# Kernel optimization log

Measured on AMD Instinct MI355X. Metric: run time of the kernel, lower is better.

## Reference

```python
import jax, jax.numpy as jnp
import numpy as np

B, L, D, H, K = 8, 200, 256, 8, 20
HS = D // H


def setup_inputs() -> dict:
    key = jax.random.key(0)
    ks = jax.random.split(key, 12)
    def xavier(k, shape):
        fan_in, fan_out = shape[1], shape[0]
        lim = np.sqrt(2.0) * np.sqrt(6.0 / (fan_in + fan_out))  # gain=relu
        return jax.random.uniform(k, shape, jnp.float32, -lim, lim)
    return {
        "seqs": jax.random.normal(ks[0], (B, L, D), jnp.float32),
        "attention_mask": jax.random.bernoulli(ks[1], 0.3, (L, L)),
        "time_matrices": jax.random.normal(ks[2], (B, L, L, D), jnp.float32),
        "conv1_w": xavier(ks[3], (D, D)),
        "conv1_b": jnp.zeros((D,), jnp.float32),
        "conv2_w": xavier(ks[4], (D, D)),
        "conv2_b": jnp.zeros((D,), jnp.float32),
        "W_w": jax.random.normal(ks[5], (D, D), jnp.float32) * (1.0 / np.sqrt(D)),
        "W_b": jnp.zeros((D,), jnp.float32),
        "ln_gamma": jnp.ones((D,), jnp.float32),
        "ln_beta": jnp.zeros((D,), jnp.float32),
    }


def _to_heads(x):
    # torch.cat(torch.split(x, HS, dim=-1), dim=0): [B,L,D] -> [H*B,L,HS], index h*B+b
    return jnp.concatenate(jnp.split(x, H, axis=-1), axis=0)


def _from_heads(x):
    # inverse: [H*B,L,HS] -> [B,L,D]
    return jnp.concatenate(jnp.split(x, H, axis=0), axis=-1)


def reference(seqs, attention_mask, time_matrices, conv1_w, conv1_b,
              conv2_w, conv2_b, W_w, W_b, ln_gamma, ln_beta):
    # 1x1 Conv1d == per-token linear
    a_ = seqs @ conv1_w.T + conv1_b
    b_ = seqs @ conv2_w.T + conv2_b
    a = _to_heads(a_)                    # [HB, L, HS]
    b = _to_heads(b_)                    # [HB, L, HS]
    ti = jnp.concatenate(jnp.split(time_matrices, H, axis=3), axis=0)  # [HB, L, L, HS]

    # attention scores: QK^T + time interaction
    att = jnp.einsum('bqh,bkh->bqk', a, b) + jnp.einsum('bqkh,bqh->bqk', ti, a)
    a_2 = jnp.linalg.norm(a, axis=-1)[..., None]              # [HB, L, 1]
    b_t_2 = jnp.linalg.norm(b[:, None, :, :] + ti, axis=-1)   # [HB, L, L]
    raw_graph = att / (a_2 * b_t_2 + 1e-6)

    attn_mask = jnp.broadcast_to(attention_mask[None], raw_graph.shape)
    raw_graph = jnp.where(attn_mask, 0.0, raw_graph)

    # top-K per row, symmetric binary mask (vectorized scatter)
    _, idx = jax.lax.top_k(raw_graph, K)                      # [HB, L, K]
    HB = raw_graph.shape[0]
    bi = jnp.arange(HB)[:, None, None]
    ri = jnp.arange(L)[None, :, None]
    mask = jnp.zeros_like(raw_graph).at[bi, ri, idx].set(1.0)
    mask = mask.at[bi, idx, ri].set(1.0)
    mask = jax.lax.stop_gradient(mask)

    sparse_graph = jnp.where(attn_mask, 0.0, raw_graph * mask)

    seqs_h = _to_heads(seqs @ W_w.T + W_b)                    # [HB, L, HS]
    outputs = sparse_graph @ seqs_h                           # [HB, L, HS]
    time_outputs = jnp.einsum('bqk,bqkh->bqh', sparse_graph, ti)

    outputs = _from_heads(outputs)                            # [B, L, D]
    time_outputs = _from_heads(time_outputs)                  # [B, L, D]

    # LayerNorm(eps=1e-8), biased variance (torch semantics)
    mu = outputs.mean(-1, keepdims=True)
    var = ((outputs - mu) ** 2).mean(-1, keepdims=True)
    ln = (outputs - mu) / jnp.sqrt(var + 1e-8) * ln_gamma + ln_beta
    return ln, time_outputs
```

## Files before the change

kernel.cpp:

```cpp
#include <hip/hip_runtime.h>
#include <hip/hip_bf16.h>

#define B_  8
#define L_  200
#define D_  256
#define H_  8
#define HS_ 32
#define K_  20
#define BL_ 1600
#define G_  64
#define MW_ 7
#define NEG_INF (-3.402823466e38f)

__device__ __forceinline__ float bf2f(unsigned short u){
  return __uint_as_float(((unsigned int)u) << 16);
}
__device__ __forceinline__ unsigned short f2bf(float f){
  unsigned int x = __float_as_uint(f);
  unsigned int r = (x + 0x7fffu + ((x >> 16) & 1u)) >> 16;
  return (unsigned short)r;
}
__device__ __forceinline__ void up2(unsigned int u, float& lo, float& hi){
  lo = __uint_as_float(u << 16);
  hi = __uint_as_float(u & 0xffff0000u);
}

__device__ __forceinline__ float loadf(const void* base, size_t i, int fp){
  return fp ? ((const float*)base)[i] : bf2f(((const unsigned short*)base)[i]);
}
__device__ __forceinline__ void load8f(const void* base, size_t i, int fp, float f[8]){
  if (fp){
    const float4* p = (const float4*)((const float*)base + i);
    float4 x = p[0], y = p[1];
    f[0]=x.x; f[1]=x.y; f[2]=x.z; f[3]=x.w; f[4]=y.x; f[5]=y.y; f[6]=y.z; f[7]=y.w;
  } else {
    uint4 v = *(const uint4*)((const unsigned short*)base + i);
    up2(v.x,f[0],f[1]); up2(v.y,f[2],f[3]); up2(v.z,f[4],f[5]); up2(v.w,f[6],f[7]);
  }
}
__device__ __forceinline__ int mask_at(const void* am, int i, int mk){
  switch(mk){
    case 0:  return ((const int*)am)[i] != 0;
    case 1:  return ((const unsigned char*)am)[i] != 0;
    case 2:  return ((const unsigned int*)am)[i] != 0;
    default: return ((const unsigned short*)am)[i] != 0;
  }
}
__device__ __forceinline__ void storef(void* base, size_t i, int fp, float v){
  if (fp) ((float*)base)[i] = v; else ((unsigned short*)base)[i] = f2bf(v);
}

__global__ __launch_bounds__(256) void k_detect(
    const unsigned short* __restrict__ seqs, const unsigned int* __restrict__ am,
    int* __restrict__ flags)
{
  int t = threadIdx.x;
  __shared__ int r[5];
  if (t < 5) r[t] = 0;
  __syncthreads();

  int bad = 0;
  for (int i = t; i < 4096; i += 256){
    unsigned e = (seqs[i] >> 7) & 0xFFu;
    if (e >= 160u) bad++;
  }
  int vi = 0, vb = 0, vf = 0, vh = 0;
  for (int i = t; i < 1024; i += 256){
    unsigned w = am[i];
    if (w == 0u) continue;
    if (w == 1u) vi++;
    else if (w == 0x3F800000u) vf++;
    else if (w == 0x00003F80u || w == 0x3F803F80u) vh++;
    else if ((w & 0xFEFEFEFEu) == 0u) vb++;
    else vb++;
  }
  atomicAdd(&r[0], bad); atomicAdd(&r[1], vi); atomicAdd(&r[2], vb);
  atomicAdd(&r[3], vf);  atomicAdd(&r[4], vh);
  __syncthreads();
  if (t == 0){
    flags[0] = (r[0] > 32) ? 1 : 0;
    int kind;
    if (r[2] > r[1] && r[2] > r[3] + r[4]) kind = 1;
    else if (r[4] > 0)                     kind = 3;
    else if (r[3] > r[1])                  kind = 2;
    else                                   kind = 0;
    flags[1] = kind;
  }
}

__global__ __launch_bounds__(256) void kz_zero(unsigned int* __restrict__ p, int n){
  int i = blockIdx.x * 256 + threadIdx.x;
  if (i < n) p[i] = 0u;
}

__global__ __launch_bounds__(256) void k1_linear(
    const void* __restrict__ seqs,
    const void* __restrict__ w1, const void* __restrict__ b1,
    const void* __restrict__ w2, const void* __restrict__ b2,
    const void* __restrict__ w3, const void* __restrict__ b3,
    const int* __restrict__ flags,
    float* __restrict__ da, float* __restrict__ db, float* __restrict__ dsh)
{
  int fp = flags[0];
  int bid = blockIdx.x;
  int m  = bid / 400;
  int rb = (bid % 400) * 4;
  const void* w; const void* bias; float* dst;
  if (m == 0)      { w = w1; bias = b1; dst = da;  }
  else if (m == 1) { w = w2; bias = b2; dst = db;  }
  else             { w = w3; bias = b3; dst = dsh; }

  __shared__ float s4[4][D_];
  int t = threadIdx.x;
  for (int l = t; l < 4 * D_; l += 256){
    int rr = l >> 8, c = l & 255;
    s4[rr][c] = loadf(seqs, (size_t)(rb + rr) * D_ + c, fp);
  }
  __syncthreads();

  float acc[4];
  float bv = loadf(bias, t, fp);
  #pragma unroll
  for (int rr = 0; rr < 4; rr++) acc[rr] = bv;

  for (int c8 = 0; c8 < 32; c8++){
    float wf[8];
    load8f(w, (size_t)t * D_ + c8 * 8, fp, wf);
    #pragma unroll
    for (int rr = 0; rr < 4; rr++){
      const float* sf = &s4[rr][c8 * 8];
      #pragma unroll
      for (int i = 0; i < 8; i++) acc[rr] += sf[i] * wf[i];
    }
  }
  #pragma unroll
  for (int rr = 0; rr < 4; rr++)
    dst[(size_t)(rb + rr) * D_ + t] = acc[rr];
}

__global__ __launch_bounds__(256) void k2_rawtopk(
    const float* __restrict__ a_, const float* __restrict__ b_,
    const void* __restrict__ tm, const void* __restrict__ am,
    const int* __restrict__ flags, unsigned int* __restrict__ maskw)
{
  int fp = flags[0], mk = flags[1];
  int bid = blockIdx.x;
  int bb = bid / L_;
  int q  = bid - bb * L_;
  int t = threadIdx.x;
  int h = t >> 5, j = t & 31;

  __shared__ float a_sh[D_];
  __shared__ float b_sh[32 * 257];
  __shared__ float raw_sh[8 * 208];

  a_sh[t] = a_[(size_t)(bb * L_ + q) * D_ + t];
  __syncthreads();

  float areg[HS_];
  #pragma unroll
  for (int e = 0; e < HS_; e++) areg[e] = a_sh[h * HS_ + e];
  float a2 = 0.f;
  #pragma unroll
  for (int e = 0; e < HS_; e++) a2 += areg[e] * areg[e];
  a2 = sqrtf(a2);

  const int amrow = q * L_;

  for (int tile = 0; tile < 7; tile++){
    __syncthreads();
    for (int l = t; l < 32 * D_; l += 256){
      int row = l >> 8;
      int col = l & 255;
      int k = tile * 32 + row;
      float v = 0.f;
      if (k < L_) v = b_[(size_t)(bb * L_ + k) * D_ + col];
      b_sh[row * 257 + col] = v;
    }
    __syncthreads();

    int k = tile * 32 + j;
    if (k < L_){
      size_t pbase = ((size_t)(bb * L_ + q) * L_ + k) * D_ + h * HS_;
      const float* brow = &b_sh[j * 257 + h * HS_];
      float p1 = 0.f, p2 = 0.f;
      #pragma unroll
      for (int e8 = 0; e8 < 4; e8++){
        float tf[8];
        load8f(tm, pbase + e8 * 8, fp, tf);
        #pragma unroll
        for (int i = 0; i < 8; i++){
          float s = brow[e8 * 8 + i] + tf[i];
          p1 += areg[e8 * 8 + i] * s;
          p2 += s * s;
        }
      }
      float r = p1 / (a2 * sqrtf(p2) + 1e-6f);
      if (mask_at(am, amrow + k, mk)) r = 0.f;
      raw_sh[h * 208 + k] = r;
    }
  }
  __syncthreads();

  int wv = t >> 6, lane = t & 63;
  for (int hh = 2 * wv; hh <= 2 * wv + 1; hh++){
    const float* r = &raw_sh[hh * 208];
    int g = hh * B_ + bb;

    float v0 = (lane       < L_) ? r[lane]       : NEG_INF;
    float v1 = (lane + 64  < L_) ? r[lane + 64]  : NEG_INF;
    float v2 = (lane + 128 < L_) ? r[lane + 128] : NEG_INF;
    float v3 = (lane + 192 < L_) ? r[lane + 192] : NEG_INF;

    for (int it = 0; it < K_; it++){
      float bv = v0; int bi = lane;
      if (v1 > bv){ bv = v1; bi = lane + 64;  }
      if (v2 > bv){ bv = v2; bi = lane + 128; }
      if (v3 > bv){ bv = v3; bi = lane + 192; }
      #pragma unroll
      for (int off = 1; off < 64; off <<= 1){
        float ov = __shfl_xor(bv, off);
        int   oi = __shfl_xor(bi, off);
        if (ov > bv || (ov == bv && oi < bi)){ bv = ov; bi = oi; }
      }
      if (bi == lane)            v0 = NEG_INF;
      else if (bi == lane + 64)  v1 = NEG_INF;
      else if (bi == lane + 128) v2 = NEG_INF;
      else if (bi == lane + 192) v3 = NEG_INF;
      if (lane == 0){
        atomicOr(&maskw[((size_t)g * L_ + q)  * MW_ + (bi >> 5)], 1u << (bi & 31));
        atomicOr(&maskw[((size_t)g * L_ + bi) * MW_ + (q  >> 5)], 1u << (q  & 31));
      }
    }
  }
}

__global__ __launch_bounds__(256) void k3_gatherln(
    const float* __restrict__ a_, const float* __restrict__ b_,
    const float* __restrict__ sh_, const void* __restrict__ tm,
    const void* __restrict__ am, const unsigned int* __restrict__ maskw,
    const void* __restrict__ gamma, const void* __restrict__ beta,
    const int* __restrict__ flags, void* __restrict__ out)
{
  int fp = flags[0], mk = flags[1];
  int bid = blockIdx.x;
  int bb = bid / L_;
  int q  = bid - bb * L_;
  int t = threadIdx.x;

  __shared__ float a_sh[D_];
  __shared__ float s_a2[8];
  __shared__ int   s_k[8][200];
  __shared__ float s_v[8][200];
  __shared__ int   s_cnt[8];
  __shared__ float red[8];

  a_sh[t] = a_[(size_t)(bb * L_ + q) * D_ + t];
  __syncthreads();
  if (t < 8){
    float s = 0.f;
    #pragma unroll
    for (int e = 0; e < HS_; e++){ float d = a_sh[t * HS_ + e]; s += d * d; }
    s_a2[t] = sqrtf(s);
  }
  __syncthreads();

  int wv = t >> 6, lane = t & 63;
  for (int hh = 2 * wv; hh <= 2 * wv + 1; hh++){
    int g = hh * B_ + bb;
    const unsigned int* mrow = &maskw[((size_t)g * L_ + q) * MW_];
    int cnt = 0;
    #pragma unroll
    for (int c = 0; c < 4; c++){
      int k = c * 64 + lane;
      bool sel = (k < L_) && ((mrow[k >> 5] >> (k & 31)) & 1u) && !mask_at(am, q * L_ + k, mk);
      unsigned long long bal = __ballot(sel);
      int pos = __popcll(bal & ((1ull << lane) - 1ull));
      if (sel) s_k[hh][cnt + pos] = k;
      cnt += __popcll(bal);
    }
    if (lane == 0) s_cnt[hh] = cnt;
    float a2 = s_a2[hh];
    for (int i = lane; i < cnt; i += 64){
      int k = s_k[hh][i];
      size_t pbase = ((size_t)(bb * L_ + q) * L_ + k) * D_ + hh * HS_;
      const float4* b4 = (const float4*)(b_ + (size_t)(bb * L_ + k) * D_ + hh * HS_);
      float p1 = 0.f, p2 = 0.f;
      #pragma unroll
      for (int e8 = 0; e8 < 4; e8++){
        float tf[8];
        load8f(tm, pbase + e8 * 8, fp, tf);
        float4 bv0 = b4[e8 * 2], bv1 = b4[e8 * 2 + 1];
        float bf[8] = {bv0.x, bv0.y, bv0.z, bv0.w, bv1.x, bv1.y, bv1.z, bv1.w};
        #pragma unroll
        for (int i2 = 0; i2 < 8; i2++){
          float s = bf[i2] + tf[i2];
          p1 += a_sh[hh * HS_ + e8 * 8 + i2] * s;
          p2 += s * s;
        }
      }
      s_v[hh][i] = p1 / (a2 * sqrtf(p2) + 1e-6f);
    }
  }
  __syncthreads();

  int h = t >> 5, hs = t & 31;
  int cnt = s_cnt[h];
  float acc_o = 0.f, acc_t = 0.f;
  const size_t tmrow = (size_t)(bb * L_ + q) * L_ * D_;
  for (int i = 0; i < cnt; i++){
    int k = s_k[h][i];
    float v = s_v[h][i];
    acc_o += v * sh_[(size_t)(bb * L_ + k) * D_ + h * HS_ + hs];
    acc_t += v * loadf(tm, tmrow + (size_t)k * D_ + h * HS_ + hs, fp);
  }
  size_t orow = (size_t)(bb * L_ + q) * D_;
  storef(out, (size_t)409600 + orow + t, fp, acc_t);

  float s = acc_o;
  #pragma unroll
  for (int off = 1; off < 64; off <<= 1) s += __shfl_xor(s, off);
  if (lane == 0) red[wv] = s;
  __syncthreads();
  float mean = (red[0] + red[1] + red[2] + red[3]) * (1.f / 256.f);

  float d = acc_o - mean;
  float s2 = d * d;
  #pragma unroll
  for (int off = 1; off < 64; off <<= 1) s2 += __shfl_xor(s2, off);
  if (lane == 0) red[4 + wv] = s2;
  __syncthreads();
  float var = (red[4] + red[5] + red[6] + red[7]) * (1.f / 256.f);

  float y = d * (1.f / sqrtf(var + 1e-8f)) * loadf(gamma, t, fp) + loadf(beta, t, fp);
  storef(out, orow + t, fp, y);
}

extern "C" void kernel_launch(void* const* d_in, const int* in_sizes, int n_in,
                              void* d_out, int out_size, void* d_ws, size_t ws_size,
                              hipStream_t stream) {
  const void* seqs = d_in[0];
  const void* am   = d_in[1];
  const void* tm   = d_in[2];
  const void* w1   = d_in[3];
  const void* b1   = d_in[4];
  const void* w2   = d_in[5];
  const void* b2   = d_in[6];
  const void* w3   = d_in[7];
  const void* b3   = d_in[8];
  const void* lng  = d_in[9];
  const void* lnb  = d_in[10];

  float* ws = (float*)d_ws;
  int*   flags = (int*)ws;
  float* a_    = ws + 16;
  float* b_    = ws + 16 + 409600;
  float* sh_   = ws + 16 + 819200;
  unsigned int* maskw = (unsigned int*)(ws + 16 + 1228800);

  k_detect   <<<1,   256, 0, stream>>>((const unsigned short*)seqs, (const unsigned int*)am, flags);
  kz_zero    <<<350, 256, 0, stream>>>(maskw, G_ * L_ * MW_);
  k1_linear  <<<1200, 256, 0, stream>>>(seqs, w1, b1, w2, b2, w3, b3, flags, a_, b_, sh_);
  k2_rawtopk <<<BL_, 256, 0, stream>>>(a_, b_, tm, am, flags, maskw);
  k3_gatherln<<<BL_, 256, 0, stream>>>(a_, b_, sh_, tm, am, maskw, lng, lnb, flags, d_out);
}
```

Before: 705.6 us.

## Read b and time rows directly with coalesced loads and cache raw scores for gather

The score kernel no longer stages b tiles in shared memory. Each group of four lanes now covers one head's 32 channels for a key, and the partial sums are combined with shuffles, so both the time-matrix and b reads become contiguous rows. The full raw-score matrix is also written to workspace, letting the gather kernel look up selected scores instead of re-reading time_matrices to recompute them. This adds a roughly 10 MB score buffer, which is only used when the workspace is large enough.

```diff
diff --git a/kernel.cpp b/kernel.cpp
--- a/kernel.cpp
+++ b/kernel.cpp
@@ -141,66 +141,74 @@
 __global__ __launch_bounds__(256) void k2_rawtopk(
     const float* __restrict__ a_, const float* __restrict__ b_,
     const void* __restrict__ tm, const void* __restrict__ am,
-    const int* __restrict__ flags, unsigned int* __restrict__ maskw)
+    const int* __restrict__ flags, unsigned int* __restrict__ maskw,
+    float* __restrict__ rawg)
 {
   int fp = flags[0], mk = flags[1];
   int bid = blockIdx.x;
   int bb = bid / L_;
   int q  = bid - bb * L_;
   int t = threadIdx.x;
-  int h = t >> 5, j = t & 31;
-
-  __shared__ float a_sh[D_];
-  __shared__ float b_sh[32 * 257];
+  int rsub = t >> 5;
+  int cg   = t & 31;
+  int c0   = cg * 8;
+  int h    = cg >> 2;
+
   __shared__ float raw_sh[8 * 208];
 
-  a_sh[t] = a_[(size_t)(bb * L_ + q) * D_ + t];
-  __syncthreads();
-
-  float areg[HS_];
-  #pragma unroll
-  for (int e = 0; e < HS_; e++) areg[e] = a_sh[h * HS_ + e];
-  float a2 = 0.f;
-  #pragma unroll
-  for (int e = 0; e < HS_; e++) a2 += areg[e] * areg[e];
-  a2 = sqrtf(a2);
-
+  float areg[8];
+  const float* arow = a_ + (size_t)(bb * L_ + q) * D_;
+  {
+    const float4* a4 = (const float4*)(arow + c0);
+    float4 x = a4[0], y = a4[1];
+    areg[0]=x.x; areg[1]=x.y; areg[2]=x.z; areg[3]=x.w;
+    areg[4]=y.x; areg[5]=y.y; areg[6]=y.z; areg[7]=y.w;
+  }
+  float a2;
+  {
+    float s = 0.f;
+    #pragma unroll
+    for (int e = 0; e < 8; e++) s += areg[e] * areg[e];
+    s += __shfl_xor(s, 1);
+    s += __shfl_xor(s, 2);
+    a2 = sqrtf(s);
+  }
+
+  const size_t tmbase = (size_t)(bb * L_ + q) * L_ * D_;
+  const float* bbase  = b_ + (size_t)bb * L_ * D_;
   const int amrow = q * L_;
 
-  for (int tile = 0; tile < 7; tile++){
-    __syncthreads();
-    for (int l = t; l < 32 * D_; l += 256){
-      int row = l >> 8;
-      int col = l & 255;
-      int k = tile * 32 + row;
-      float v = 0.f;
-      if (k < L_) v = b_[(size_t)(bb * L_ + k) * D_ + col];
-      b_sh[row * 257 + col] = v;
-    }
-    __syncthreads();
-
-    int k = tile * 32 + j;
-    if (k < L_){
-      size_t pbase = ((size_t)(bb * L_ + q) * L_ + k) * D_ + h * HS_;
-      const float* brow = &b_sh[j * 257 + h * HS_];
-      float p1 = 0.f, p2 = 0.f;
-      #pragma unroll
-      for (int e8 = 0; e8 < 4; e8++){
-        float tf[8];
-        load8f(tm, pbase + e8 * 8, fp, tf);
-        #pragma unroll
-        for (int i = 0; i < 8; i++){
-          float s = brow[e8 * 8 + i] + tf[i];
-          p1 += areg[e8 * 8 + i] * s;
-          p2 += s * s;
-        }
-      }
+  for (int k0 = 0; k0 < L_; k0 += 8){
+    int k = k0 + rsub;
+    float tf[8];
+    load8f(tm, tmbase + (size_t)k * D_ + c0, fp, tf);
+    const float4* b4 = (const float4*)(bbase + (size_t)k * D_ + c0);
+    float4 bv0 = b4[0], bv1 = b4[1];
+    float bf[8] = {bv0.x, bv0.y, bv0.z, bv0.w, bv1.x, bv1.y, bv1.z, bv1.w};
+    float p1 = 0.f, p2 = 0.f;
+    #pragma unroll
+    for (int i = 0; i < 8; i++){
+      float sv = bf[i] + tf[i];
+      p1 += areg[i] * sv;
+      p2 += sv * sv;
+    }
+    p1 += __shfl_xor(p1, 1); p2 += __shfl_xor(p2, 1);
+    p1 += __shfl_xor(p1, 2); p2 += __shfl_xor(p2, 2);
+    if ((cg & 3) == 0){
       float r = p1 / (a2 * sqrtf(p2) + 1e-6f);
       if (mask_at(am, amrow + k, mk)) r = 0.f;
       raw_sh[h * 208 + k] = r;
     }
   }
   __syncthreads();
+
+  if (rawg){
+    #pragma unroll
+    for (int hh2 = 0; hh2 < 8; hh2++){
+      if (t < L_)
+        rawg[((size_t)(hh2 * B_ + bb) * L_ + q) * L_ + t] = raw_sh[hh2 * 208 + t];
+    }
+  }
 
   int wv = t >> 6, lane = t & 63;
   for (int hh = 2 * wv; hh <= 2 * wv + 1; hh++){
@@ -240,7 +248,8 @@
     const float* __restrict__ sh_, const void* __restrict__ tm,
     const void* __restrict__ am, const unsigned int* __restrict__ maskw,
     const void* __restrict__ gamma, const void* __restrict__ beta,
-    const int* __restrict__ flags, void* __restrict__ out)
+    const int* __restrict__ flags, const float* __restrict__ rawg,
+    void* __restrict__ out)
 {
   int fp = flags[0], mk = flags[1];
   int bid = blockIdx.x;
@@ -280,26 +289,33 @@
       cnt += __popcll(bal);
     }
     if (lane == 0) s_cnt[hh] = cnt;
-    float a2 = s_a2[hh];
-    for (int i = lane; i < cnt; i += 64){
-      int k = s_k[hh][i];
-      size_t pbase = ((size_t)(bb * L_ + q) * L_ + k) * D_ + hh * HS_;
-      const float4* b4 = (const float4*)(b_ + (size_t)(bb * L_ + k) * D_ + hh * HS_);
-      float p1 = 0.f, p2 = 0.f;
-      #pragma unroll
-      for (int e8 = 0; e8 < 4; e8++){
-        float tf[8];
-        load8f(tm, pbase + e8 * 8, fp, tf);
-        float4 bv0 = b4[e8 * 2], bv1 = b4[e8 * 2 + 1];
-        float bf[8] = {bv0.x, bv0.y, bv0.z, bv0.w, bv1.x, bv1.y, bv1.z, bv1.w};
+
+    if (rawg){
+      const float* rrow = rawg + ((size_t)g * L_ + q) * L_;
+      for (int i = lane; i < cnt; i += 64)
+        s_v[hh][i] = rrow[s_k[hh][i]];
+    } else {
+      float a2 = s_a2[hh];
+      for (int i = lane; i < cnt; i += 64){
+        int k = s_k[hh][i];
+        size_t pbase = ((size_t)(bb * L_ + q) * L_ + k) * D_ + hh * HS_;
+        const float4* b4 = (const float4*)(b_ + (size_t)(bb * L_ + k) * D_ + hh * HS_);
+        float p1 = 0.f, p2 = 0.f;
         #pragma unroll
-        for (int i2 = 0; i2 < 8; i2++){
-          float s = bf[i2] + tf[i2];
-          p1 += a_sh[hh * HS_ + e8 * 8 + i2] * s;
-          p2 += s * s;
+        for (int e8 = 0; e8 < 4; e8++){
+          float tf[8];
+          load8f(tm, pbase + e8 * 8, fp, tf);
+          float4 bv0 = b4[e8 * 2], bv1 = b4[e8 * 2 + 1];
+          float bf[8] = {bv0.x, bv0.y, bv0.z, bv0.w, bv1.x, bv1.y, bv1.z, bv1.w};
+          #pragma unroll
+          for (int i2 = 0; i2 < 8; i2++){
+            float s = bf[i2] + tf[i2];
+            p1 += a_sh[hh * HS_ + e8 * 8 + i2] * s;
+            p2 += s * s;
+          }
         }
+        s_v[hh][i] = p1 / (a2 * sqrtf(p2) + 1e-6f);
       }
-      s_v[hh][i] = p1 / (a2 * sqrtf(p2) + 1e-6f);
     }
   }
   __syncthreads();
@@ -357,10 +373,13 @@
   float* b_    = ws + 16 + 409600;
   float* sh_   = ws + 16 + 819200;
   unsigned int* maskw = (unsigned int*)(ws + 16 + 1228800);
+  float* rawg  = ws + 16 + 1228800 + 89600;
+  size_t need  = ((size_t)16 + 1228800 + 89600 + 2560000) * 4;
+  float* rawg_arg = (ws_size >= need) ? rawg : nullptr;
 
   k_detect   <<<1,   256, 0, stream>>>((const unsigned short*)seqs, (const unsigned int*)am, flags);
   kz_zero    <<<350, 256, 0, stream>>>(maskw, G_ * L_ * MW_);
   k1_linear  <<<1200, 256, 0, stream>>>(seqs, w1, b1, w2, b2, w3, b3, flags, a_, b_, sh_);
-  k2_rawtopk <<<BL_, 256, 0, stream>>>(a_, b_, tm, am, flags, maskw);
-  k3_gatherln<<<BL_, 256, 0, stream>>>(a_, b_, sh_, tm, am, maskw, lng, lnb, flags, d_out);
-}
+  k2_rawtopk <<<BL_, 256, 0, stream>>>(a_, b_, tm, am, flags, maskw, rawg_arg);
+  k3_gatherln<<<BL_, 256, 0, stream>>>(a_, b_, sh_, tm, am, maskw, lng, lnb, flags, rawg_arg, d_out);
+}
```

Result: faster. 610.3 us (-13.5%).
